# Kernel optimization log

Hardware: AMD Instinct MI355X
Metric: run time of the kernel (lower is better)

## Reference

```python
import jax, jax.numpy as jnp
import numpy as np

BIG = 1.0e8  # masked_fill value from the torch module


def setup_inputs() -> dict:
    key = jax.random.key(0)
    k1, k2, k3, k4 = jax.random.split(key, 4)
    B, N, M, D = 32, 2048, 2048, 3
    o_weights = jax.random.randint(k1, (B, N), 0, 2, dtype=jnp.int32)
    outputs = jax.random.normal(k2, (B, N, D), dtype=jnp.float32)
    t_weights = jax.random.randint(k3, (B, M), 0, 2, dtype=jnp.int32)
    targets = jax.random.normal(k4, (B, M, D), dtype=jnp.float32)
    return {"o_weights": o_weights, "outputs": outputs, "t_weights": t_weights, "targets": targets}


def _chamfer(mask_a, pc_a, mask_b, pc_b):
    # pairwise Euclidean distances [B, N, M] via ||a||^2 + ||b||^2 - 2 a.b
    a2 = jnp.sum(pc_a * pc_a, axis=-1)  # [B, N]
    b2 = jnp.sum(pc_b * pc_b, axis=-1)  # [B, M]
    ab = jnp.einsum("bnd,bmd->bnm", pc_a, pc_b)
    d2 = jnp.maximum(a2[..., :, None] + b2[..., None, :] - 2.0 * ab, 0.0)
    dist = jnp.sqrt(d2)  # [B, N, M]
    mm = (mask_a != 0)[..., :, None] & (mask_b != 0)[..., None, :]
    dist = jnp.where(mm, dist, BIG)
    ma = mask_a.astype(pc_a.dtype)
    mb = mask_b.astype(pc_b.dtype)
    min1 = jnp.min(dist, axis=-1) ** 2 * ma  # [B, N]
    min2 = jnp.min(dist, axis=-2) ** 2 * mb  # [B, M]
    return 0.5 * (jnp.sum(min1, axis=-1) + jnp.sum(min2, axis=-1))  # [B]


def reference(o_weights, outputs, t_weights, targets):
    return _chamfer(o_weights, outputs, t_weights, targets)
```

## Files before the change

kernel.cpp:

```cpp
#include <hip/hip_runtime.h>
#include <hip/hip_bf16.h>

#define B_    32
#define N_    2048
#define M_    2048
#define RW_   8
#define GX_   32
#define BIG2  1.0e16f

typedef float v2f __attribute__((ext_vector_type(2)));

__device__ __forceinline__ v2f v2_fma(v2f a, v2f b, v2f c) {
#if __has_builtin(__builtin_elementwise_fma)
    return __builtin_elementwise_fma(a, b, c);
#else
    v2f r; r.x = fmaf(a.x, b.x, c.x); r.y = fmaf(a.y, b.y, c.y); return r;
#endif
}
__device__ __forceinline__ v2f v2_min(v2f a, v2f b) {
#if __has_builtin(__builtin_elementwise_min)
    return __builtin_elementwise_min(a, b);
#else
    v2f r; r.x = fminf(a.x, b.x); r.y = fminf(a.y, b.y); return r;
#endif
}

__global__ __launch_bounds__(512, 8) void chamfer_main(
    const int* __restrict__ o_w, const float* __restrict__ o_pts,
    const int* __restrict__ t_w, const float* __restrict__ t_pts,
    float* __restrict__ partials)
{
    const int dir  = blockIdx.z;
    const int b    = blockIdx.y;
    const int tid  = threadIdx.x;
    const int lane = tid & 63;
    const int wv   = tid >> 6;
    const int row0 = blockIdx.x * (8 * RW_) + wv * RW_;

    const int*   wa; const float* pa;
    const int*   wb; const float* pb;
    if (dir == 0) { wa = o_w; pa = o_pts; wb = t_w; pb = t_pts; }
    else          { wa = t_w; pa = t_pts; wb = o_w; pb = o_pts; }

    __shared__ float4 sq[M_];
    __shared__ float  wsum[8];

    {
        const float2* src2 = (const float2*)(pb + (size_t)b * M_ * 3);
        const int2*   wb2  = (const int2*)(wb + (size_t)b * M_);
        #pragma unroll
        for (int k = 0; k < 2; ++k) {
            int p = tid + k * 512;
            float2 u0 = src2[p * 3 + 0];
            float2 u1 = src2[p * 3 + 1];
            float2 u2 = src2[p * 3 + 2];
            int2   mm = wb2[p];
            float x0 = u0.x, y0 = u0.y, z0 = u1.x;
            float x1 = u1.y, y1 = u2.x, z1 = u2.y;
            float n20 = fmaf(x0, x0, fmaf(y0, y0, z0 * z0));
            float n21 = fmaf(x1, x1, fmaf(y1, y1, z1 * z1));
            sq[2 * p]     = make_float4(-2.f * x0, -2.f * y0, -2.f * z0,
                                        mm.x ? n20 : BIG2);
            sq[2 * p + 1] = make_float4(-2.f * x1, -2.f * y1, -2.f * z1,
                                        mm.y ? n21 : BIG2);
        }
    }

    v2f rx2[4], ry2[4], rz2[4];
    {
        const float* rp = pa + (size_t)(b * N_ + row0) * 3;
        #pragma unroll
        for (int j = 0; j < 4; ++j) {
            rx2[j] = (v2f){ rp[(2 * j) * 3 + 0], rp[(2 * j + 1) * 3 + 0] };
            ry2[j] = (v2f){ rp[(2 * j) * 3 + 1], rp[(2 * j + 1) * 3 + 1] };
            rz2[j] = (v2f){ rp[(2 * j) * 3 + 2], rp[(2 * j + 1) * 3 + 2] };
        }
    }
    __syncthreads();

    v2f acc[4];
    #pragma unroll
    for (int j = 0; j < 4; ++j) acc[j] = (v2f){ 3.4e38f, 3.4e38f };

    #pragma unroll 2
    for (int t = 0; t < M_ / 64; ++t) {
        float4 q = sq[t * 64 + lane];
        v2f qx = (v2f){ q.x, q.x };
        v2f qy = (v2f){ q.y, q.y };
        v2f qz = (v2f){ q.z, q.z };
        v2f qw = (v2f){ q.w, q.w };
        #pragma unroll
        for (int j = 0; j < 4; ++j) {
            v2f d = v2_fma(rx2[j], qx, v2_fma(ry2[j], qy, v2_fma(rz2[j], qz, qw)));
            acc[j] = v2_min(acc[j], d);
        }
    }

    const int* wp = wa + (size_t)b * N_ + row0;
    float sum = 0.0f;
    #pragma unroll
    for (int j = 0; j < 4; ++j) {
        float m0 = acc[j].x, m1 = acc[j].y;
        #pragma unroll
        for (int off = 32; off; off >>= 1) {
            m0 = fminf(m0, __shfl_xor(m0, off, 64));
            m1 = fminf(m1, __shfl_xor(m1, off, 64));
        }
        float a20 = fmaf(rx2[j].x, rx2[j].x,
                    fmaf(ry2[j].x, ry2[j].x, rz2[j].x * rz2[j].x));
        float a21 = fmaf(rx2[j].y, rx2[j].y,
                    fmaf(ry2[j].y, ry2[j].y, rz2[j].y * rz2[j].y));
        float d20 = fmaxf(a20 + m0, 0.0f);
        float d21 = fmaxf(a21 + m1, 0.0f);
        sum += (wp[2 * j]     != 0) ? d20 : 0.0f;
        sum += (wp[2 * j + 1] != 0) ? d21 : 0.0f;
    }
    if (lane == 0) wsum[wv] = sum;
    __syncthreads();
    if (tid == 0) {
        float s = 0.f;
        #pragma unroll
        for (int i = 0; i < 8; ++i) s += wsum[i];
        partials[((size_t)b * 2 + dir) * GX_ + blockIdx.x] = s;
    }
}

__global__ __launch_bounds__(256) void chamfer_finish(
    const float* __restrict__ partials, float* __restrict__ loss)
{
    int t = threadIdx.x;
    int b = t >> 3, k = t & 7;
    const float4* p4 = (const float4*)(partials + b * (2 * GX_) + k * 8);
    float4 u = p4[0], v = p4[1];
    float s = ((u.x + u.y) + (u.z + u.w)) + ((v.x + v.y) + (v.z + v.w));
    #pragma unroll
    for (int off = 4; off; off >>= 1) s += __shfl_xor(s, off, 64);
    if (k == 0) loss[b] = 0.5f * s;
}

__global__ void chamfer_zero(float* __restrict__ loss)
{
    if (threadIdx.x < B_) loss[threadIdx.x] = 0.0f;
}

__global__ __launch_bounds__(256) void chamfer_nolds(
    const int* __restrict__ o_w, const float* __restrict__ o_pts,
    const int* __restrict__ t_w, const float* __restrict__ t_pts,
    float* __restrict__ loss)
{
    const int dir  = blockIdx.z;
    const int b    = blockIdx.y;
    const int lane = threadIdx.x & 63;
    const int wv   = threadIdx.x >> 6;
    const int row0 = (blockIdx.x * 4 + wv) * 16;

    const int*   __restrict__ wa = (dir == 0) ? o_w   : t_w;
    const float* __restrict__ pa = (dir == 0) ? o_pts : t_pts;
    const int*   __restrict__ wb = (dir == 0) ? t_w   : o_w;
    const float* __restrict__ pb = (dir == 0) ? t_pts : o_pts;

    int base = __builtin_amdgcn_readfirstlane((b * N_ + row0) * 3);
    const float* rp = pa + base;
    float rx[16], ry[16], rz[16];
    #pragma unroll
    for (int r = 0; r < 16; ++r) {
        rx[r] = rp[3 * r + 0];
        ry[r] = rp[3 * r + 1];
        rz[r] = rp[3 * r + 2];
    }
    float acc[16];
    #pragma unroll
    for (int r = 0; r < 16; ++r) acc[r] = 3.4e38f;

    #pragma unroll 2
    for (int t = 0; t < M_ / 64; ++t) {
        int ib = b * M_ + t * 64 + lane;
        float bx = pb[ib * 3 + 0], by = pb[ib * 3 + 1], bz = pb[ib * 3 + 2];
        float n2 = fmaf(bx, bx, fmaf(by, by, bz * bz));
        float qw = (wb[ib] != 0) ? n2 : BIG2;
        float qx = -2.0f * bx, qy = -2.0f * by, qz = -2.0f * bz;
        #pragma unroll
        for (int r = 0; r < 16; ++r) {
            float d = fmaf(rx[r], qx, fmaf(ry[r], qy, fmaf(rz[r], qz, qw)));
            acc[r] = fminf(acc[r], d);
        }
    }
    #pragma unroll
    for (int r = 0; r < 16; ++r) {
        float v = acc[r];
        #pragma unroll
        for (int off = 32; off; off >>= 1) v = fminf(v, __shfl_xor(v, off, 64));
        acc[r] = v;
    }
    int mbase = __builtin_amdgcn_readfirstlane(b * N_ + row0);
    const int* wp = wa + mbase;
    float sum = 0.0f;
    #pragma unroll
    for (int r = 0; r < 16; ++r) {
        float a2 = fmaf(rx[r], rx[r], fmaf(ry[r], ry[r], rz[r] * rz[r]));
        float d2 = fmaxf(a2 + acc[r], 0.0f);
        sum += (wp[r] != 0) ? d2 : 0.0f;
    }
    if (lane == 0) atomicAdd(&loss[b], 0.5f * sum);
}

extern "C" void kernel_launch(void* const* d_in, const int* in_sizes, int n_in,
                              void* d_out, int out_size, void* d_ws, size_t ws_size,
                              hipStream_t stream) {
    const int*   o_w   = (const int*)  d_in[0];
    const float* o_pts = (const float*)d_in[1];
    const int*   t_w   = (const int*)  d_in[2];
    const float* t_pts = (const float*)d_in[3];
    float* loss = (float*)d_out;

    const size_t part_bytes = (size_t)B_ * 2 * GX_ * sizeof(float);

    if (ws_size >= part_bytes) {
        float* partials = (float*)d_ws;
        dim3 grid(GX_, B_, 2);
        chamfer_main<<<grid, 512, 0, stream>>>(
            o_w, o_pts, t_w, t_pts, partials);
        chamfer_finish<<<1, 256, 0, stream>>>(partials, loss);
    } else {
        chamfer_zero<<<1, 64, 0, stream>>>(loss);
        dim3 grid(N_ / 64, B_, 2);
        chamfer_nolds<<<grid, 256, 0, stream>>>(
            o_w, o_pts, t_w, t_pts, loss);
    }
}
```

Measured before the change: 90.81 us.

## Pack two query points per v2f lane in split LDS arrays with software prefetch

The shared query buffer is split into two float4 arrays laid out SoA-style, so each lane handles two query points per v2f operation while each row coordinate is splatted. The row-wise min reduction now folds the two halves before the cross-lane shuffle, halving shuffle work. The loop runs half as many iterations and prefetches the next LDS entry into registers, and the launch-bounds occupancy hint is dropped. This should cut LDS reads per FMA and overlap LDS latency with compute, at the cost of extra registers for the prefetch buffers.

```diff
diff --git a/kernel.cpp b/kernel.cpp
--- a/kernel.cpp
+++ b/kernel.cpp
@@ -24,8 +24,11 @@
     v2f r; r.x = fminf(a.x, b.x); r.y = fminf(a.y, b.y); return r;
 #endif
 }
-
-__global__ __launch_bounds__(512, 8) void chamfer_main(
+__device__ __forceinline__ v2f v2_splat(float s) { return (v2f){ s, s }; }
+
+union F4V2 { float4 f4; struct { v2f lo, hi; } v; };
+
+__global__ __launch_bounds__(512) void chamfer_main(
     const int* __restrict__ o_w, const float* __restrict__ o_pts,
     const int* __restrict__ t_w, const float* __restrict__ t_pts,
     float* __restrict__ partials)
@@ -42,7 +45,8 @@
     if (dir == 0) { wa = o_w; pa = o_pts; wb = t_w; pb = t_pts; }
     else          { wa = t_w; pa = t_pts; wb = o_w; pb = o_pts; }
 
-    __shared__ float4 sq[M_];
+    __shared__ float4 sqA[M_ / 2];
+    __shared__ float4 sqB[M_ / 2];
     __shared__ float  wsum[8];
 
     {
@@ -59,61 +63,59 @@
             float x1 = u1.y, y1 = u2.x, z1 = u2.y;
             float n20 = fmaf(x0, x0, fmaf(y0, y0, z0 * z0));
             float n21 = fmaf(x1, x1, fmaf(y1, y1, z1 * z1));
-            sq[2 * p]     = make_float4(-2.f * x0, -2.f * y0, -2.f * z0,
-                                        mm.x ? n20 : BIG2);
-            sq[2 * p + 1] = make_float4(-2.f * x1, -2.f * y1, -2.f * z1,
-                                        mm.y ? n21 : BIG2);
-        }
-    }
-
-    v2f rx2[4], ry2[4], rz2[4];
-    {
-        const float* rp = pa + (size_t)(b * N_ + row0) * 3;
-        #pragma unroll
-        for (int j = 0; j < 4; ++j) {
-            rx2[j] = (v2f){ rp[(2 * j) * 3 + 0], rp[(2 * j + 1) * 3 + 0] };
-            ry2[j] = (v2f){ rp[(2 * j) * 3 + 1], rp[(2 * j + 1) * 3 + 1] };
-            rz2[j] = (v2f){ rp[(2 * j) * 3 + 2], rp[(2 * j + 1) * 3 + 2] };
-        }
+            sqA[p] = make_float4(-2.f * x0, -2.f * x1, -2.f * y0, -2.f * y1);
+            sqB[p] = make_float4(-2.f * z0, -2.f * z1,
+                                 mm.x ? n20 : BIG2, mm.y ? n21 : BIG2);
+        }
+    }
+
+    int base = __builtin_amdgcn_readfirstlane((b * N_ + row0) * 3);
+    const float* rp = pa + base;
+    float rx[RW_], ry[RW_], rz[RW_];
+    #pragma unroll
+    for (int r = 0; r < RW_; ++r) {
+        rx[r] = rp[3 * r + 0];
+        ry[r] = rp[3 * r + 1];
+        rz[r] = rp[3 * r + 2];
     }
     __syncthreads();
 
-    v2f acc[4];
-    #pragma unroll
-    for (int j = 0; j < 4; ++j) acc[j] = (v2f){ 3.4e38f, 3.4e38f };
-
-    #pragma unroll 2
-    for (int t = 0; t < M_ / 64; ++t) {
-        float4 q = sq[t * 64 + lane];
-        v2f qx = (v2f){ q.x, q.x };
-        v2f qy = (v2f){ q.y, q.y };
-        v2f qz = (v2f){ q.z, q.z };
-        v2f qw = (v2f){ q.w, q.w };
-        #pragma unroll
-        for (int j = 0; j < 4; ++j) {
-            v2f d = v2_fma(rx2[j], qx, v2_fma(ry2[j], qy, v2_fma(rz2[j], qz, qw)));
-            acc[j] = v2_min(acc[j], d);
-        }
-    }
-
-    const int* wp = wa + (size_t)b * N_ + row0;
+    v2f acc[RW_];
+    #pragma unroll
+    for (int r = 0; r < RW_; ++r) acc[r] = v2_splat(3.4e38f);
+
+    F4V2 qa, qb, na, nb;
+    qa.f4 = sqA[lane];
+    qb.f4 = sqB[lane];
+    #pragma unroll 4
+    for (int t = 0; t < M_ / 128; ++t) {
+        if (t + 1 < M_ / 128) {
+            na.f4 = sqA[(t + 1) * 64 + lane];
+            nb.f4 = sqB[(t + 1) * 64 + lane];
+        }
+        v2f xs = qa.v.lo, ys = qa.v.hi, zs = qb.v.lo, ws = qb.v.hi;
+        #pragma unroll
+        for (int r = 0; r < RW_; ++r) {
+            v2f d = v2_fma(v2_splat(rx[r]), xs,
+                    v2_fma(v2_splat(ry[r]), ys,
+                    v2_fma(v2_splat(rz[r]), zs, ws)));
+            acc[r] = v2_min(acc[r], d);
+        }
+        qa = na; qb = nb;
+    }
+
+    int mbase = __builtin_amdgcn_readfirstlane(b * N_ + row0);
+    const int* wp = wa + mbase;
     float sum = 0.0f;
     #pragma unroll
-    for (int j = 0; j < 4; ++j) {
-        float m0 = acc[j].x, m1 = acc[j].y;
-        #pragma unroll
-        for (int off = 32; off; off >>= 1) {
-            m0 = fminf(m0, __shfl_xor(m0, off, 64));
-            m1 = fminf(m1, __shfl_xor(m1, off, 64));
-        }
-        float a20 = fmaf(rx2[j].x, rx2[j].x,
-                    fmaf(ry2[j].x, ry2[j].x, rz2[j].x * rz2[j].x));
-        float a21 = fmaf(rx2[j].y, rx2[j].y,
-                    fmaf(ry2[j].y, ry2[j].y, rz2[j].y * rz2[j].y));
-        float d20 = fmaxf(a20 + m0, 0.0f);
-        float d21 = fmaxf(a21 + m1, 0.0f);
-        sum += (wp[2 * j]     != 0) ? d20 : 0.0f;
-        sum += (wp[2 * j + 1] != 0) ? d21 : 0.0f;
+    for (int r = 0; r < RW_; ++r) {
+        float m = fminf(acc[r].x, acc[r].y);
+        #pragma unroll
+        for (int off = 32; off; off >>= 1)
+            m = fminf(m, __shfl_xor(m, off, 64));
+        float a2 = fmaf(rx[r], rx[r], fmaf(ry[r], ry[r], rz[r] * rz[r]));
+        float d2 = fmaxf(a2 + m, 0.0f);
+        sum += (wp[r] != 0) ? d2 : 0.0f;
     }
     if (lane == 0) wsum[wv] = sum;
     __syncthreads();
```

New measurement: 85.29 us. -6.1%, faster.

## Compute chamfer distances with bf16 MFMA using hi/lo split precision

Applied to the files above, without the earlier changes.

Replaces the FP32 FMA distance loop with MFMA 16x16x32 bf16 matrix ops. A prep kernel packs each target point into hi/lo bf16 pairs (-2x, -2y, -2z, masked norm) so a single MFMA yields ||b||^2 - 2a·b with near-fp32 accuracy. The main kernel then takes row minima over the MFMA output tiles. This moves the dominant arithmetic onto the matrix units. The cost is an extra prep kernel, a workspace round trip, and half the lanes loading zeros. Split-bf16 error could slightly perturb the minima compared with fp32.

```diff
diff --git a/kernel.cpp b/kernel.cpp
--- a/kernel.cpp
+++ b/kernel.cpp
@@ -4,125 +4,135 @@
 #define B_    32
 #define N_    2048
 #define M_    2048
-#define RW_   8
-#define GX_   32
 #define BIG2  1.0e16f
 
-typedef float v2f __attribute__((ext_vector_type(2)));
-
-__device__ __forceinline__ v2f v2_fma(v2f a, v2f b, v2f c) {
-#if __has_builtin(__builtin_elementwise_fma)
-    return __builtin_elementwise_fma(a, b, c);
-#else
-    v2f r; r.x = fmaf(a.x, b.x, c.x); r.y = fmaf(a.y, b.y, c.y); return r;
-#endif
-}
-__device__ __forceinline__ v2f v2_min(v2f a, v2f b) {
-#if __has_builtin(__builtin_elementwise_min)
-    return __builtin_elementwise_min(a, b);
-#else
-    v2f r; r.x = fminf(a.x, b.x); r.y = fminf(a.y, b.y); return r;
-#endif
-}
-
-__global__ __launch_bounds__(512, 8) void chamfer_main(
+typedef float f32x4  __attribute__((ext_vector_type(4)));
+typedef short bf16x8 __attribute__((ext_vector_type(8)));
+
+__device__ __forceinline__ short f2bf(float f) {
+    unsigned u = __float_as_uint(f);
+    u = (u + 0x7FFFu + ((u >> 16) & 1u)) >> 16;
+    return (short)u;
+}
+__device__ __forceinline__ float bf2f(short s) {
+    return __uint_as_float(((unsigned)(unsigned short)s) << 16);
+}
+
+__global__ __launch_bounds__(256) void chamfer_prep_mfma(
     const int* __restrict__ o_w, const float* __restrict__ o_pts,
     const int* __restrict__ t_w, const float* __restrict__ t_pts,
-    float* __restrict__ partials)
-{
-    const int dir  = blockIdx.z;
-    const int b    = blockIdx.y;
+    char* __restrict__ wsB)
+{
+    int idx = blockIdx.x * 256 + threadIdx.x;
+    int dir = idx >> 16;
+    int r   = idx & 65535;
+    int b   = r >> 11;
+    int m   = r & 2047;
+    const int*   w = (dir == 0) ? t_w   : o_w;
+    const float* p = (dir == 0) ? t_pts : o_pts;
+    float x = p[r * 3 + 0], y = p[r * 3 + 1], z = p[r * 3 + 2];
+    float b2 = fmaf(x, x, fmaf(y, y, z * z));
+    float w2 = (w[r] != 0) ? b2 : BIG2;
+    float nx = -2.f * x, ny = -2.f * y, nz = -2.f * z;
+    short xh = f2bf(nx), yh = f2bf(ny), zh = f2bf(nz);
+    short xl = f2bf(nx - bf2f(xh));
+    short yl = f2bf(ny - bf2f(yh));
+    short zl = f2bf(nz - bf2f(zh));
+    short wh = f2bf(w2);
+    short wl = f2bf(w2 - bf2f(wh));
+    bf16x8 o0 = { xh, yh, zh, xl, yl, zl, xh, yh };
+    bf16x8 o1 = { zh, wh, wl, 0, 0, 0, 0, 0 };
+    char* base = wsB + (size_t)(b * 2 + dir) * 65536 + (size_t)m * 16;
+    *(bf16x8*)(base)         = o0;
+    *(bf16x8*)(base + 32768) = o1;
+}
+
+__global__ __launch_bounds__(512) void chamfer_mfma(
+    const int* __restrict__ o_w, const float* __restrict__ o_pts,
+    const int* __restrict__ t_w, const float* __restrict__ t_pts,
+    const char* __restrict__ wsB, float* __restrict__ partials)
+{
+    const int part = blockIdx.x, b = blockIdx.y, dir = blockIdx.z;
     const int tid  = threadIdx.x;
-    const int lane = tid & 63;
-    const int wv   = tid >> 6;
-    const int row0 = blockIdx.x * (8 * RW_) + wv * RW_;
-
-    const int*   wa; const float* pa;
-    const int*   wb; const float* pb;
-    if (dir == 0) { wa = o_w; pa = o_pts; wb = t_w; pb = t_pts; }
-    else          { wa = t_w; pa = t_pts; wb = o_w; pb = o_pts; }
-
-    __shared__ float4 sq[M_];
-    __shared__ float  wsum[8];
-
-    {
-        const float2* src2 = (const float2*)(pb + (size_t)b * M_ * 3);
-        const int2*   wb2  = (const int2*)(wb + (size_t)b * M_);
-        #pragma unroll
-        for (int k = 0; k < 2; ++k) {
-            int p = tid + k * 512;
-            float2 u0 = src2[p * 3 + 0];
-            float2 u1 = src2[p * 3 + 1];
-            float2 u2 = src2[p * 3 + 2];
-            int2   mm = wb2[p];
-            float x0 = u0.x, y0 = u0.y, z0 = u1.x;
-            float x1 = u1.y, y1 = u2.x, z1 = u2.y;
-            float n20 = fmaf(x0, x0, fmaf(y0, y0, z0 * z0));
-            float n21 = fmaf(x1, x1, fmaf(y1, y1, z1 * z1));
-            sq[2 * p]     = make_float4(-2.f * x0, -2.f * y0, -2.f * z0,
-                                        mm.x ? n20 : BIG2);
-            sq[2 * p + 1] = make_float4(-2.f * x1, -2.f * y1, -2.f * z1,
-                                        mm.y ? n21 : BIG2);
-        }
-    }
-
-    v2f rx2[4], ry2[4], rz2[4];
-    {
-        const float* rp = pa + (size_t)(b * N_ + row0) * 3;
+    const int lane = tid & 63, wv = tid >> 6;
+    const int q    = lane >> 4, c15 = lane & 15;
+
+    const float* pa = (dir == 0) ? o_pts : t_pts;
+    const int*   wa = (dir == 0) ? o_w   : t_w;
+    const int rowBase = part * 512 + wv * 64;
+
+    const short BONE = 0x3F80;
+    bf16x8 af[4];
+    #pragma unroll
+    for (int rt = 0; rt < 4; ++rt) {
+        int gi = b * N_ + rowBase + rt * 16 + c15;
+        float ax = pa[gi * 3 + 0], ay = pa[gi * 3 + 1], az = pa[gi * 3 + 2];
+        short xh = f2bf(ax), yh = f2bf(ay), zh = f2bf(az);
+        short xl = f2bf(ax - bf2f(xh));
+        short yl = f2bf(ay - bf2f(yh));
+        short zl = f2bf(az - bf2f(zh));
+        bf16x8 f0 = { xh, yh, zh, xh, yh, zh, xl, yl };
+        bf16x8 f1 = { zl, BONE, BONE, 0, 0, 0, 0, 0 };
+        bf16x8 fz = { 0, 0, 0, 0, 0, 0, 0, 0 };
+        af[rt] = (q == 0) ? f0 : ((q == 1) ? f1 : fz);
+    }
+
+    const char* bbase = wsB + (size_t)(b * 2 + dir) * 65536
+                      + (q == 1 ? 32768 : 0) + c15 * 16;
+
+    f32x4 acc[4];
+    #pragma unroll
+    for (int rt = 0; rt < 4; ++rt)
+        acc[rt] = (f32x4){ 3.4e38f, 3.4e38f, 3.4e38f, 3.4e38f };
+    const f32x4 CZERO = (f32x4){ 0.f, 0.f, 0.f, 0.f };
+
+    #pragma unroll 4
+    for (int ct = 0; ct < 128; ++ct) {
+        bf16x8 bf = { 0, 0, 0, 0, 0, 0, 0, 0 };
+        if (lane < 32)
+            bf = *(const bf16x8*)(bbase + ct * 256);
+        #pragma unroll
+        for (int rt = 0; rt < 4; ++rt) {
+            f32x4 d = __builtin_amdgcn_mfma_f32_16x16x32_bf16(
+                          af[rt], bf, CZERO, 0, 0, 0);
+            acc[rt][0] = fminf(acc[rt][0], d[0]);
+            acc[rt][1] = fminf(acc[rt][1], d[1]);
+            acc[rt][2] = fminf(acc[rt][2], d[2]);
+            acc[rt][3] = fminf(acc[rt][3], d[3]);
+        }
+    }
+
+    #pragma unroll
+    for (int rt = 0; rt < 4; ++rt) {
         #pragma unroll
         for (int j = 0; j < 4; ++j) {
-            rx2[j] = (v2f){ rp[(2 * j) * 3 + 0], rp[(2 * j + 1) * 3 + 0] };
-            ry2[j] = (v2f){ rp[(2 * j) * 3 + 1], rp[(2 * j + 1) * 3 + 1] };
-            rz2[j] = (v2f){ rp[(2 * j) * 3 + 2], rp[(2 * j + 1) * 3 + 2] };
-        }
-    }
-    __syncthreads();
-
-    v2f acc[4];
-    #pragma unroll
-    for (int j = 0; j < 4; ++j) acc[j] = (v2f){ 3.4e38f, 3.4e38f };
-
-    #pragma unroll 2
-    for (int t = 0; t < M_ / 64; ++t) {
-        float4 q = sq[t * 64 + lane];
-        v2f qx = (v2f){ q.x, q.x };
-        v2f qy = (v2f){ q.y, q.y };
-        v2f qz = (v2f){ q.z, q.z };
-        v2f qw = (v2f){ q.w, q.w };
-        #pragma unroll
-        for (int j = 0; j < 4; ++j) {
-            v2f d = v2_fma(rx2[j], qx, v2_fma(ry2[j], qy, v2_fma(rz2[j], qz, qw)));
-            acc[j] = v2_min(acc[j], d);
-        }
-    }
-
-    const int* wp = wa + (size_t)b * N_ + row0;
-    float sum = 0.0f;
-    #pragma unroll
-    for (int j = 0; j < 4; ++j) {
-        float m0 = acc[j].x, m1 = acc[j].y;
-        #pragma unroll
-        for (int off = 32; off; off >>= 1) {
-            m0 = fminf(m0, __shfl_xor(m0, off, 64));
-            m1 = fminf(m1, __shfl_xor(m1, off, 64));
-        }
-        float a20 = fmaf(rx2[j].x, rx2[j].x,
-                    fmaf(ry2[j].x, ry2[j].x, rz2[j].x * rz2[j].x));
-        float a21 = fmaf(rx2[j].y, rx2[j].y,
-                    fmaf(ry2[j].y, ry2[j].y, rz2[j].y * rz2[j].y));
-        float d20 = fmaxf(a20 + m0, 0.0f);
-        float d21 = fmaxf(a21 + m1, 0.0f);
-        sum += (wp[2 * j]     != 0) ? d20 : 0.0f;
-        sum += (wp[2 * j + 1] != 0) ? d21 : 0.0f;
-    }
-    if (lane == 0) wsum[wv] = sum;
-    __syncthreads();
-    if (tid == 0) {
-        float s = 0.f;
-        #pragma unroll
-        for (int i = 0; i < 8; ++i) s += wsum[i];
-        partials[((size_t)b * 2 + dir) * GX_ + blockIdx.x] = s;
-    }
+            float v = acc[rt][j];
+            v = fminf(v, __shfl_xor(v, 1, 64));
+            v = fminf(v, __shfl_xor(v, 2, 64));
+            v = fminf(v, __shfl_xor(v, 4, 64));
+            v = fminf(v, __shfl_xor(v, 8, 64));
+            acc[rt][j] = v;
+        }
+    }
+
+    float sum = 0.f;
+    if (c15 == 0) {
+        #pragma unroll
+        for (int rt = 0; rt < 4; ++rt) {
+            #pragma unroll
+            for (int j = 0; j < 4; ++j) {
+                int gi = b * N_ + rowBase + rt * 16 + q * 4 + j;
+                float ax = pa[gi * 3 + 0], ay = pa[gi * 3 + 1], az = pa[gi * 3 + 2];
+                float a2 = fmaf(ax, ax, fmaf(ay, ay, az * az));
+                float d2 = fmaxf(a2 + acc[rt][j], 0.f);
+                sum += (wa[gi] != 0) ? d2 : 0.f;
+            }
+        }
+    }
+    #pragma unroll
+    for (int off = 32; off; off >>= 1) sum += __shfl_xor(sum, off, 64);
+    if (lane == 0)
+        partials[b * 64 + dir * 32 + part * 8 + wv] = sum;
 }
 
 __global__ __launch_bounds__(256) void chamfer_finish(
@@ -130,7 +140,7 @@
 {
     int t = threadIdx.x;
     int b = t >> 3, k = t & 7;
-    const float4* p4 = (const float4*)(partials + b * (2 * GX_) + k * 8);
+    const float4* p4 = (const float4*)(partials + b * 64 + k * 8);
     float4 u = p4[0], v = p4[1];
     float s = ((u.x + u.y) + (u.z + u.w)) + ((v.x + v.y) + (v.z + v.w));
     #pragma unroll
@@ -213,13 +223,16 @@
     const float* t_pts = (const float*)d_in[3];
     float* loss = (float*)d_out;
 
-    const size_t part_bytes = (size_t)B_ * 2 * GX_ * sizeof(float);
-
-    if (ws_size >= part_bytes) {
-        float* partials = (float*)d_ws;
-        dim3 grid(GX_, B_, 2);
-        chamfer_main<<<grid, 512, 0, stream>>>(
-            o_w, o_pts, t_w, t_pts, partials);
+    const size_t bBytes    = (size_t)64 * 65536;
+    const size_t partBytes = 2048 * sizeof(float);
+
+    if (ws_size >= bBytes + partBytes) {
+        char*  wsB      = (char*)d_ws;
+        float* partials = (float*)((char*)d_ws + bBytes);
+        chamfer_prep_mfma<<<512, 256, 0, stream>>>(
+            o_w, o_pts, t_w, t_pts, wsB);
+        chamfer_mfma<<<dim3(4, B_, 2), 512, 0, stream>>>(
+            o_w, o_pts, t_w, t_pts, wsB, partials);
         chamfer_finish<<<1, 256, 0, stream>>>(partials, loss);
     } else {
         chamfer_zero<<<1, 64, 0, stream>>>(loss);
```

Result: slower. 107.7 us (+18.6%).
